# Kernel optimization log

Hardware: AMD Instinct MI355X
Metric: run time of the kernel (lower is better)

Reference implementation:

```python
import jax, jax.numpy as jnp
import numpy as np

ALPHA = 1.702  # sigmoid-GLU scale
LIMIT = 7.0    # clamp limit
TOP_K = 2      # num_experts_per_tok


def setup_inputs() -> dict:
    key = jax.random.key(0)
    ks = jax.random.split(key, 4)
    B, S, H, E, I = 2, 1024, 1024, 8, 2048
    return {
        "hidden_states": jax.random.normal(ks[0], (B, S, H), jnp.float32),
        "router_weight": jax.random.normal(ks[1], (E, H), jnp.float32),
        "router_bias": jnp.zeros((E,), jnp.float32),
        "gate_up_proj": jax.random.normal(ks[2], (E, H, 2 * I), jnp.float32) * 0.02,
        "gate_up_bias": jnp.zeros((E, 2 * I), jnp.float32),
        "down_proj": jax.random.normal(ks[3], (E, I, H), jnp.float32) * 0.02,
        "down_bias": jnp.zeros((E, H), jnp.float32),
    }


def reference(hidden_states, router_weight, router_bias, gate_up_proj,
              gate_up_bias, down_proj, down_bias):
    B, S, H = hidden_states.shape
    E, _, two_I = gate_up_proj.shape
    I = two_I // 2

    flat = hidden_states.reshape(B * S, H)  # [T, H]

    # Router: softmax + top-k
    logits = flat @ router_weight.T + router_bias            # [T, E]
    scores = jax.nn.softmax(logits, axis=-1)
    topk_w, topk_idx = jax.lax.top_k(scores, TOP_K)          # [T, K]

    # Dense per-expert gated FFN (einsum 'abmh,ehn->abemn' computes all experts
    # on all tokens; the reshape/permute dance is a mathematical no-op).
    gu = jnp.einsum('th,ehn->ten', flat, gate_up_proj) + gate_up_bias  # [T, E, 2I]
    gate = jnp.minimum(gu[..., :I], LIMIT)
    up = jnp.clip(gu[..., I:], -LIMIT, LIMIT)
    glu = gate * jax.nn.sigmoid(gate * ALPHA)
    act = (up + 1.0) * glu                                   # [T, E, I]

    down = jnp.einsum('tei,eih->teh', act, down_proj) + down_bias  # [T, E, H]

    # Combine: gather each token's top-k expert outputs, weighted sum.
    gathered = jnp.take_along_axis(down, topk_idx[:, :, None], axis=1)  # [T, K, H]
    out = (gathered * topk_w[:, :, None]).sum(axis=1)        # [T, H]
    return out.reshape(B, S, H)
```

## Files before the change

kernel.cpp:

```cpp
#include <hip/hip_runtime.h>
#include <math.h>

#define TT 2048
#define HH 1024
#define EE 8
#define II 2048
#define N1 4096
#define ALPHA 1.702f
#define LIMIT 7.0f
#define MAXSCHED 40

typedef __attribute__((ext_vector_type(8))) short short8;
typedef __attribute__((ext_vector_type(4))) float floatx4;

#define GLL(g, l) __builtin_amdgcn_global_load_lds(                          \
    (const __attribute__((address_space(1))) void*)(g),                      \
    (__attribute__((address_space(3))) void*)(l), 16, 0, 0)

__device__ __forceinline__ short f2bf(float f) {
  union { float f; unsigned u; } v; v.f = f;
  unsigned r = (v.u + 0x7fffu + ((v.u >> 16) & 1u)) >> 16;
  return (short)r;
}
__device__ __forceinline__ float bf2f(unsigned short s) {
  union { unsigned u; float f; } v; v.u = ((unsigned)s) << 16;
  return v.f;
}

__global__ __launch_bounds__(256) void convert_x(const float* __restrict__ x,
                                                 unsigned short* __restrict__ xb) {
  const size_t off = ((size_t)blockIdx.x * blockDim.x + threadIdx.x) * 8;
  const float4 v0 = *(const float4*)(x + off);
  const float4 v1 = *(const float4*)(x + off + 4);
  short8 s;
  s[0]=f2bf(v0.x); s[1]=f2bf(v0.y); s[2]=f2bf(v0.z); s[3]=f2bf(v0.w);
  s[4]=f2bf(v1.x); s[5]=f2bf(v1.y); s[6]=f2bf(v1.z); s[7]=f2bf(v1.w);
  *(short8*)(xb + off) = s;
}

__global__ __launch_bounds__(256) void router_kernel(
    const float* __restrict__ x, const float* __restrict__ rw,
    const float* __restrict__ rb, int* __restrict__ topk_idx,
    float* __restrict__ topk_w) {
  const int t = blockIdx.x;
  const float* xr = x + (size_t)t * HH;
  const int lane = threadIdx.x & 63;
  const int wave = threadIdx.x >> 6;
  float xv[16];
#pragma unroll
  for (int i = 0; i < 16; i++) xv[i] = xr[lane + i * 64];
  __shared__ float logits[EE];
#pragma unroll
  for (int ee = 0; ee < 2; ee++) {
    const int e = wave * 2 + ee;
    const float* wr = rw + (size_t)e * HH;
    float s = 0.f;
#pragma unroll
    for (int i = 0; i < 16; i++) s += xv[i] * wr[lane + i * 64];
#pragma unroll
    for (int off = 32; off > 0; off >>= 1) s += __shfl_down(s, off, 64);
    if (lane == 0) logits[e] = s + rb[e];
  }
  __syncthreads();
  if (threadIdx.x == 0) {
    float sc[EE];
    float mx = -3.4e38f;
    for (int i = 0; i < EE; i++) mx = fmaxf(mx, logits[i]);
    float sum = 0.f;
    for (int i = 0; i < EE; i++) { sc[i] = expf(logits[i] - mx); sum += sc[i]; }
    const float inv = 1.f / sum;
    int i0 = 0;
    for (int i = 1; i < EE; i++) if (sc[i] > sc[i0]) i0 = i;
    int i1 = (i0 == 0) ? 1 : 0;
    for (int i = 0; i < EE; i++) if (i != i0 && sc[i] > sc[i1]) i1 = i;
    topk_idx[t * 2 + 0] = i0;
    topk_idx[t * 2 + 1] = i1;
    topk_w[t * 2 + 0] = sc[i0] * inv;
    topk_w[t * 2 + 1] = sc[i1] * inv;
  }
}

__global__ void assign_kernel(const int* __restrict__ topk_idx,
                              int* __restrict__ counts, int* __restrict__ rows) {
  const int id = blockIdx.x * blockDim.x + threadIdx.x;
  if (id >= TT * 2) return;
  const int e = topk_idx[id];
  const int slot = atomicAdd(&counts[e], 1);
  rows[e * TT + slot] = id;
}

__global__ void sched_kernel(const int* __restrict__ counts,
                             int* __restrict__ sched, int* __restrict__ nsched) {
  if (threadIdx.x == 0) {
    int n = 0;
    for (int e = 0; e < EE; e++) {
      const int mt = (counts[e] + 127) >> 7;
      for (int m = 0; m < mt; m++) sched[n++] = (e << 8) | m;
    }
    nsched[0] = n;
  }
}

__global__ __launch_bounds__(256, 3) void gemm_gu(
    const unsigned short* __restrict__ x_bf,
    const float* __restrict__ gup,
    const float* __restrict__ gub,
    const int* __restrict__ counts, const int* __restrict__ rows,
    const int* __restrict__ sched, const int* __restrict__ nsched,
    unsigned short* __restrict__ gu) {
  const int sid = blockIdx.y;
  if (sid >= nsched[0]) return;
  const int sv = sched[sid];
  const int e = sv >> 8, mtile = sv & 255;
  const int count = counts[e] - mtile * 128;
  const int ntile = blockIdx.x;
  const int* rl = rows + e * TT + mtile * 128;

  __shared__ short As[128 * 128];

  const int tid = threadIdx.x;
  const int lane = tid & 63, wave = tid >> 6;
  const int quad = lane >> 4, r16 = lane & 15;
  const int wm = (wave & 1) << 6, wn = (wave >> 1) << 6;

  const unsigned short* asrc[8];
#pragma unroll
  for (int p = 0; p < 8; p++) {
    const int m = wave * 32 + p * 4 + (lane >> 4);
    const int cm = (m < count) ? m : 0;
    const int g = (lane & 15) ^ (m & 15);
    asrc[p] = x_bf + (size_t)(rl[cm] >> 1) * HH + g * 8;
  }

  const int nbase = ntile * 128 + wn + r16;
  int voff[8];
#pragma unroll
  for (int j = 0; j < 8; j++) voff[j] = (quad * 8 + j) * N1 + nbase;
  const float* bbase = gup + (size_t)e * HH * N1;

  floatx4 acc[4][4] = {};

  for (int c = 0; c < 8; c++) {
    __syncthreads();
#pragma unroll
    for (int p = 0; p < 8; p++)
      GLL(asrc[p] + c * 128, &As[(wave * 32 + p * 4) * 128]);
    __syncthreads();
#pragma unroll 2
    for (int kt = 0; kt < 4; kt++) {
      short8 af[4];
#pragma unroll
      for (int i = 0; i < 4; i++) {
        const int m = wm + i * 16 + r16;
        const int sl = (kt * 4 + quad) ^ r16;
        af[i] = *(const short8*)&As[m * 128 + sl * 8];
      }
#pragma unroll
      for (int f = 0; f < 4; f++) {
        float bv[8];
#pragma unroll
        for (int j = 0; j < 8; j++) bv[j] = bbase[voff[j] + f * 16];
        union { unsigned u[4]; short8 s8; } bp;
#pragma unroll
        for (int j = 0; j < 4; j++)
          bp.u[j] = __builtin_amdgcn_perm(__float_as_uint(bv[2 * j + 1]),
                                          __float_as_uint(bv[2 * j]), 0x07060302u);
#pragma unroll
        for (int i = 0; i < 4; i++)
          acc[i][f] = __builtin_amdgcn_mfma_f32_16x16x32_bf16(af[i], bp.s8, acc[i][f], 0, 0, 0);
      }
#pragma unroll
      for (int j = 0; j < 8; j++) voff[j] += 32 * N1;
    }
  }

  const float* bias = gub + (size_t)e * N1 + ntile * 128;
#pragma unroll
  for (int i = 0; i < 4; i++) {
#pragma unroll
    for (int reg = 0; reg < 4; reg++) {
      const int rrow = wm + i * 16 + quad * 4 + reg;
      if (rrow < count) {
        const int ent = rl[rrow];
        unsigned short* orow = gu + (size_t)ent * N1 + ntile * 128;
#pragma unroll
        for (int f = 0; f < 4; f++) {
          const int cc = wn + f * 16 + r16;
          orow[cc] = (unsigned short)f2bf(acc[i][f][reg] + bias[cc]);
        }
      }
    }
  }
}

__global__ __launch_bounds__(256) void act_kernel(const unsigned short* __restrict__ gu,
                                                  unsigned short* __restrict__ act) {
  const int id = blockIdx.x * blockDim.x + threadIdx.x;
  const int r = id >> 8;
  const int i8 = (id & 255) * 8;
  const short8 g8 = *(const short8*)(gu + (size_t)r * N1 + i8);
  const short8 u8 = *(const short8*)(gu + (size_t)r * N1 + II + i8);
  short8 o;
#pragma unroll
  for (int j = 0; j < 8; j++) {
    float g = bf2f((unsigned short)g8[j]);
    float u = bf2f((unsigned short)u8[j]);
    g = fminf(g, LIMIT);
    u = fminf(fmaxf(u, -LIMIT), LIMIT);
    const float glu = g / (1.f + expf(-g * ALPHA));
    o[j] = f2bf((u + 1.f) * glu);
  }
  *(short8*)(act + (size_t)r * II + i8) = o;
}

__global__ __launch_bounds__(256, 3) void gemm_down(
    const unsigned short* __restrict__ act,
    const float* __restrict__ dp,
    const int* __restrict__ counts, const int* __restrict__ rows,
    const int* __restrict__ sched, const int* __restrict__ nsched,
    float* __restrict__ dout) {
  const int sid = blockIdx.y;
  if (sid >= nsched[0]) return;
  const int sv = sched[sid];
  const int e = sv >> 8, mtile = sv & 255;
  const int count = counts[e] - mtile * 128;
  const int ntile = blockIdx.x;
  const int kbase = blockIdx.z * (II / 4);
  const int* rl = rows + e * TT + mtile * 128;

  __shared__ short As[128 * 128];

  const int tid = threadIdx.x;
  const int lane = tid & 63, wave = tid >> 6;
  const int quad = lane >> 4, r16 = lane & 15;
  const int wm = (wave & 1) << 6, wn = (wave >> 1) << 6;

  const unsigned short* asrc[8];
#pragma unroll
  for (int p = 0; p < 8; p++) {
    const int m = wave * 32 + p * 4 + (lane >> 4);
    const int cm = (m < count) ? m : 0;
    const int g = (lane & 15) ^ (m & 15);
    asrc[p] = act + (size_t)rl[cm] * II + kbase + g * 8;
  }

  const int nbase = ntile * 128 + wn + r16;
  int voff[8];
#pragma unroll
  for (int j = 0; j < 8; j++) voff[j] = (kbase + quad * 8 + j) * HH + nbase;
  const float* bbase = dp + (size_t)e * II * HH;

  floatx4 acc[4][4] = {};

  for (int c = 0; c < 4; c++) {
    __syncthreads();
#pragma unroll
    for (int p = 0; p < 8; p++)
      GLL(asrc[p] + c * 128, &As[(wave * 32 + p * 4) * 128]);
    __syncthreads();
#pragma unroll 2
    for (int kt = 0; kt < 4; kt++) {
      short8 af[4];
#pragma unroll
      for (int i = 0; i < 4; i++) {
        const int m = wm + i * 16 + r16;
        const int sl = (kt * 4 + quad) ^ r16;
        af[i] = *(const short8*)&As[m * 128 + sl * 8];
      }
#pragma unroll
      for (int f = 0; f < 4; f++) {
        float bv[8];
#pragma unroll
        for (int j = 0; j < 8; j++) bv[j] = bbase[voff[j] + f * 16];
        union { unsigned u[4]; short8 s8; } bp;
#pragma unroll
        for (int j = 0; j < 4; j++)
          bp.u[j] = __builtin_amdgcn_perm(__float_as_uint(bv[2 * j + 1]),
                                          __float_as_uint(bv[2 * j]), 0x07060302u);
#pragma unroll
        for (int i = 0; i < 4; i++)
          acc[i][f] = __builtin_amdgcn_mfma_f32_16x16x32_bf16(af[i], bp.s8, acc[i][f], 0, 0, 0);
      }
#pragma unroll
      for (int j = 0; j < 8; j++) voff[j] += 32 * HH;
    }
  }

#pragma unroll
  for (int i = 0; i < 4; i++) {
#pragma unroll
    for (int reg = 0; reg < 4; reg++) {
      const int rrow = wm + i * 16 + quad * 4 + reg;
      if (rrow < count) {
        const int ent = rl[rrow];
        float* orow = dout + (size_t)ent * HH + ntile * 128;
#pragma unroll
        for (int f = 0; f < 4; f++) {
          const int cc = wn + f * 16 + r16;
          atomicAdd(&orow[cc], acc[i][f][reg]);
        }
      }
    }
  }
}

__global__ __launch_bounds__(256) void combine_kernel(
    const float* __restrict__ dout, const float* __restrict__ tw,
    const int* __restrict__ tidx, const float* __restrict__ db,
    float* __restrict__ out) {
  const int id = blockIdx.x * blockDim.x + threadIdx.x;
  const int t = id >> 8;
  const int h = (id & 255) * 4;
  const float w0 = tw[t * 2], w1 = tw[t * 2 + 1];
  const int e0 = tidx[t * 2], e1 = tidx[t * 2 + 1];
  const float4 a = *(const float4*)(dout + (size_t)(2 * t) * HH + h);
  const float4 b = *(const float4*)(dout + (size_t)(2 * t + 1) * HH + h);
  const float4 b0 = *(const float4*)(db + (size_t)e0 * HH + h);
  const float4 b1 = *(const float4*)(db + (size_t)e1 * HH + h);
  float4 o;
  o.x = w0 * (a.x + b0.x) + w1 * (b.x + b1.x);
  o.y = w0 * (a.y + b0.y) + w1 * (b.y + b1.y);
  o.z = w0 * (a.z + b0.z) + w1 * (b.z + b1.z);
  o.w = w0 * (a.w + b0.w) + w1 * (b.w + b1.w);
  *(float4*)(out + (size_t)t * HH + h) = o;
}

extern "C" void kernel_launch(void* const* d_in, const int* in_sizes, int n_in,
                              void* d_out, int out_size, void* d_ws, size_t ws_size,
                              hipStream_t stream) {
  const float* x   = (const float*)d_in[0];
  const float* rw  = (const float*)d_in[1];
  const float* rb  = (const float*)d_in[2];
  const float* gup = (const float*)d_in[3];
  const float* gub = (const float*)d_in[4];
  const float* dp  = (const float*)d_in[5];
  const float* db  = (const float*)d_in[6];
  float* out = (float*)d_out;

  char* ws = (char*)d_ws;
  int*   topk_idx = (int*)(ws + 0);
  float* topk_w   = (float*)(ws + 16384);
  int*   counts   = (int*)(ws + 32768);
  int*   nsched   = (int*)(ws + 33024);
  int*   sched    = (int*)(ws + 33280);
  int*   rows     = (int*)(ws + 36864);
  unsigned short* x_bf = (unsigned short*)(ws + (1u << 20));
  unsigned short* gu   = (unsigned short*)(ws + 8388608);
  unsigned short* act  = (unsigned short*)(ws + 50331648);
  float*          dout = (float*)(ws + 75497472);

  convert_x<<<TT * HH / (256 * 8), 256, 0, stream>>>(x, x_bf);
  router_kernel<<<TT, 256, 0, stream>>>(x, rw, rb, topk_idx, topk_w);
  hipMemsetAsync(counts, 0, 64, stream);
  assign_kernel<<<(TT * 2 + 255) / 256, 256, 0, stream>>>(topk_idx, counts, rows);
  sched_kernel<<<1, 64, 0, stream>>>(counts, sched, nsched);
  gemm_gu<<<dim3(N1 / 128, MAXSCHED), 256, 0, stream>>>(
      x_bf, gup, gub, counts, rows, sched, nsched, gu);
  act_kernel<<<TT * 2 * II / (256 * 8), 256, 0, stream>>>(gu, act);
  hipMemsetAsync(dout, 0, (size_t)TT * 2 * HH * 4, stream);
  gemm_down<<<dim3(HH / 128, MAXSCHED, 4), 256, 0, stream>>>(
      act, dp, counts, rows, sched, nsched, dout);
  combine_kernel<<<(TT * HH / 4) / 256, 256, 0, stream>>>(dout, topk_w, topk_idx, db, out);
}
```

Before: 457.2 us.

## Fuse GLU activation into gate-up GEMM, use 32x32 MFMA, drop split-K atomics

The gate-up GEMM now tiles 64 gate columns and the matching 64 up columns together, so the clamp and sigmoid-GLU run in its epilogue. This removes the separate activation kernel and the bf16 round-trip of the gate/up buffer. Both GEMMs switch from 16x16x32 to 32x32x16 bf16 MFMA with a 2x2 accumulator layout. Split-K partials in the down GEMM are written to separate slices and summed in the combine kernel, replacing atomics and the memset at the cost of more combine-time memory reads. Occupancy hints rise to 4 blocks per SIMD group.

After: 495.0 us. 8.3% more time.

```diff
diff --git a/kernel.cpp b/kernel.cpp
--- a/kernel.cpp
+++ b/kernel.cpp
@@ -9,9 +9,10 @@
 #define ALPHA 1.702f
 #define LIMIT 7.0f
 #define MAXSCHED 40
+#define SPLITK 4
 
 typedef __attribute__((ext_vector_type(8))) short short8;
-typedef __attribute__((ext_vector_type(4))) float floatx4;
+typedef __attribute__((ext_vector_type(16))) float floatx16;
 
 #define GLL(g, l) __builtin_amdgcn_global_load_lds(                          \
     (const __attribute__((address_space(1))) void*)(g),                      \
@@ -101,13 +102,13 @@
   }
 }
 
-__global__ __launch_bounds__(256, 3) void gemm_gu(
+__global__ __launch_bounds__(256, 4) void gemm_gu(
     const unsigned short* __restrict__ x_bf,
     const float* __restrict__ gup,
     const float* __restrict__ gub,
     const int* __restrict__ counts, const int* __restrict__ rows,
     const int* __restrict__ sched, const int* __restrict__ nsched,
-    unsigned short* __restrict__ gu) {
+    unsigned short* __restrict__ act) {
   const int sid = blockIdx.y;
   if (sid >= nsched[0]) return;
   const int sv = sched[sid];
@@ -120,8 +121,9 @@
 
   const int tid = threadIdx.x;
   const int lane = tid & 63, wave = tid >> 6;
-  const int quad = lane >> 4, r16 = lane & 15;
-  const int wm = (wave & 1) << 6, wn = (wave >> 1) << 6;
+  const int half = lane >> 5, n32 = lane & 31;
+  const int wm = (wave & 1) << 6;
+  const int wh = (wave >> 1) << 5;
 
   const unsigned short* asrc[8];
 #pragma unroll
@@ -132,13 +134,11 @@
     asrc[p] = x_bf + (size_t)(rl[cm] >> 1) * HH + g * 8;
   }
 
-  const int nbase = ntile * 128 + wn + r16;
-  int voff[8];
-#pragma unroll
-  for (int j = 0; j < 8; j++) voff[j] = (quad * 8 + j) * N1 + nbase;
+  const int acol = wh + n32;
+  const int colf[2] = { ntile * 64 + acol, II + ntile * 64 + acol };
   const float* bbase = gup + (size_t)e * HH * N1;
 
-  floatx4 acc[4][4] = {};
+  floatx16 acc[2][2] = {};
 
   for (int c = 0; c < 8; c++) {
     __syncthreads();
@@ -147,73 +147,53 @@
       GLL(asrc[p] + c * 128, &As[(wave * 32 + p * 4) * 128]);
     __syncthreads();
 #pragma unroll 2
-    for (int kt = 0; kt < 4; kt++) {
-      short8 af[4];
-#pragma unroll
-      for (int i = 0; i < 4; i++) {
-        const int m = wm + i * 16 + r16;
-        const int sl = (kt * 4 + quad) ^ r16;
+    for (int kt = 0; kt < 8; kt++) {
+      short8 af[2];
+#pragma unroll
+      for (int i = 0; i < 2; i++) {
+        const int m = wm + i * 32 + n32;
+        const int sl = (kt * 2 + half) ^ (m & 15);
         af[i] = *(const short8*)&As[m * 128 + sl * 8];
       }
-#pragma unroll
-      for (int f = 0; f < 4; f++) {
+      const float* bp0 = bbase + (size_t)(c * 128 + kt * 16 + half * 8) * N1;
+#pragma unroll
+      for (int nf = 0; nf < 2; nf++) {
         float bv[8];
 #pragma unroll
-        for (int j = 0; j < 8; j++) bv[j] = bbase[voff[j] + f * 16];
+        for (int j = 0; j < 8; j++) bv[j] = bp0[j * N1 + colf[nf]];
         union { unsigned u[4]; short8 s8; } bp;
 #pragma unroll
         for (int j = 0; j < 4; j++)
           bp.u[j] = __builtin_amdgcn_perm(__float_as_uint(bv[2 * j + 1]),
                                           __float_as_uint(bv[2 * j]), 0x07060302u);
 #pragma unroll
-        for (int i = 0; i < 4; i++)
-          acc[i][f] = __builtin_amdgcn_mfma_f32_16x16x32_bf16(af[i], bp.s8, acc[i][f], 0, 0, 0);
-      }
-#pragma unroll
-      for (int j = 0; j < 8; j++) voff[j] += 32 * N1;
-    }
-  }
-
-  const float* bias = gub + (size_t)e * N1 + ntile * 128;
-#pragma unroll
-  for (int i = 0; i < 4; i++) {
-#pragma unroll
-    for (int reg = 0; reg < 4; reg++) {
-      const int rrow = wm + i * 16 + quad * 4 + reg;
-      if (rrow < count) {
-        const int ent = rl[rrow];
-        unsigned short* orow = gu + (size_t)ent * N1 + ntile * 128;
-#pragma unroll
-        for (int f = 0; f < 4; f++) {
-          const int cc = wn + f * 16 + r16;
-          orow[cc] = (unsigned short)f2bf(acc[i][f][reg] + bias[cc]);
-        }
-      }
-    }
-  }
-}
-
-__global__ __launch_bounds__(256) void act_kernel(const unsigned short* __restrict__ gu,
-                                                  unsigned short* __restrict__ act) {
-  const int id = blockIdx.x * blockDim.x + threadIdx.x;
-  const int r = id >> 8;
-  const int i8 = (id & 255) * 8;
-  const short8 g8 = *(const short8*)(gu + (size_t)r * N1 + i8);
-  const short8 u8 = *(const short8*)(gu + (size_t)r * N1 + II + i8);
-  short8 o;
-#pragma unroll
-  for (int j = 0; j < 8; j++) {
-    float g = bf2f((unsigned short)g8[j]);
-    float u = bf2f((unsigned short)u8[j]);
-    g = fminf(g, LIMIT);
-    u = fminf(fmaxf(u, -LIMIT), LIMIT);
-    const float glu = g / (1.f + expf(-g * ALPHA));
-    o[j] = f2bf((u + 1.f) * glu);
-  }
-  *(short8*)(act + (size_t)r * II + i8) = o;
-}
-
-__global__ __launch_bounds__(256, 3) void gemm_down(
+        for (int i = 0; i < 2; i++)
+          acc[i][nf] = __builtin_amdgcn_mfma_f32_32x32x16_bf16(af[i], bp.s8, acc[i][nf], 0, 0, 0);
+      }
+    }
+  }
+
+  const float bg = gub[(size_t)e * N1 + ntile * 64 + acol];
+  const float bu = gub[(size_t)e * N1 + II + ntile * 64 + acol];
+#pragma unroll
+  for (int i = 0; i < 2; i++) {
+#pragma unroll
+    for (int reg = 0; reg < 16; reg++) {
+      const int r = wm + i * 32 + (reg & 3) + 8 * (reg >> 2) + 4 * half;
+      if (r < count) {
+        const int ent = rl[r];
+        float g = acc[i][0][reg] + bg;
+        float u = acc[i][1][reg] + bu;
+        g = fminf(g, LIMIT);
+        u = fminf(fmaxf(u, -LIMIT), LIMIT);
+        const float glu = g / (1.f + expf(-g * ALPHA));
+        act[(size_t)ent * II + ntile * 64 + acol] = (unsigned short)f2bf((u + 1.f) * glu);
+      }
+    }
+  }
+}
+
+__global__ __launch_bounds__(256, 4) void gemm_down(
     const unsigned short* __restrict__ act,
     const float* __restrict__ dp,
     const int* __restrict__ counts, const int* __restrict__ rows,
@@ -225,15 +205,17 @@
   const int e = sv >> 8, mtile = sv & 255;
   const int count = counts[e] - mtile * 128;
   const int ntile = blockIdx.x;
-  const int kbase = blockIdx.z * (II / 4);
+  const int split = blockIdx.z;
+  const int kbase = split * (II / SPLITK);
   const int* rl = rows + e * TT + mtile * 128;
 
   __shared__ short As[128 * 128];
 
   const int tid = threadIdx.x;
   const int lane = tid & 63, wave = tid >> 6;
-  const int quad = lane >> 4, r16 = lane & 15;
-  const int wm = (wave & 1) << 6, wn = (wave >> 1) << 6;
+  const int half = lane >> 5, n32 = lane & 31;
+  const int wm = (wave & 1) << 6;
+  const int wn = (wave >> 1) << 6;
 
   const unsigned short* asrc[8];
 #pragma unroll
@@ -244,61 +226,55 @@
     asrc[p] = act + (size_t)rl[cm] * II + kbase + g * 8;
   }
 
-  const int nbase = ntile * 128 + wn + r16;
-  int voff[8];
-#pragma unroll
-  for (int j = 0; j < 8; j++) voff[j] = (kbase + quad * 8 + j) * HH + nbase;
+  const int colf[2] = { ntile * 128 + wn + n32, ntile * 128 + wn + 32 + n32 };
   const float* bbase = dp + (size_t)e * II * HH;
 
-  floatx4 acc[4][4] = {};
-
-  for (int c = 0; c < 4; c++) {
+  floatx16 acc[2][2] = {};
+
+  for (int c = 0; c < II / SPLITK / 128; c++) {
     __syncthreads();
 #pragma unroll
     for (int p = 0; p < 8; p++)
       GLL(asrc[p] + c * 128, &As[(wave * 32 + p * 4) * 128]);
     __syncthreads();
 #pragma unroll 2
-    for (int kt = 0; kt < 4; kt++) {
-      short8 af[4];
-#pragma unroll
-      for (int i = 0; i < 4; i++) {
-        const int m = wm + i * 16 + r16;
-        const int sl = (kt * 4 + quad) ^ r16;
+    for (int kt = 0; kt < 8; kt++) {
+      short8 af[2];
+#pragma unroll
+      for (int i = 0; i < 2; i++) {
+        const int m = wm + i * 32 + n32;
+        const int sl = (kt * 2 + half) ^ (m & 15);
         af[i] = *(const short8*)&As[m * 128 + sl * 8];
       }
-#pragma unroll
-      for (int f = 0; f < 4; f++) {
+      const float* bp0 = bbase + (size_t)(kbase + c * 128 + kt * 16 + half * 8) * HH;
+#pragma unroll
+      for (int nf = 0; nf < 2; nf++) {
         float bv[8];
 #pragma unroll
-        for (int j = 0; j < 8; j++) bv[j] = bbase[voff[j] + f * 16];
+        for (int j = 0; j < 8; j++) bv[j] = bp0[j * HH + colf[nf]];
         union { unsigned u[4]; short8 s8; } bp;
 #pragma unroll
         for (int j = 0; j < 4; j++)
           bp.u[j] = __builtin_amdgcn_perm(__float_as_uint(bv[2 * j + 1]),
                                           __float_as_uint(bv[2 * j]), 0x07060302u);
 #pragma unroll
-        for (int i = 0; i < 4; i++)
-          acc[i][f] = __builtin_amdgcn_mfma_f32_16x16x32_bf16(af[i], bp.s8, acc[i][f], 0, 0, 0);
-      }
-#pragma unroll
-      for (int j = 0; j < 8; j++) voff[j] += 32 * HH;
-    }
-  }
-
-#pragma unroll
-  for (int i = 0; i < 4; i++) {
-#pragma unroll
-    for (int reg = 0; reg < 4; reg++) {
-      const int rrow = wm + i * 16 + quad * 4 + reg;
-      if (rrow < count) {
-        const int ent = rl[rrow];
-        float* orow = dout + (size_t)ent * HH + ntile * 128;
-#pragma unroll
-        for (int f = 0; f < 4; f++) {
-          const int cc = wn + f * 16 + r16;
-          atomicAdd(&orow[cc], acc[i][f][reg]);
-        }
+        for (int i = 0; i < 2; i++)
+          acc[i][nf] = __builtin_amdgcn_mfma_f32_32x32x16_bf16(af[i], bp.s8, acc[i][nf], 0, 0, 0);
+      }
+    }
+  }
+
+  float* dsl = dout + (size_t)split * (TT * 2) * HH;
+#pragma unroll
+  for (int i = 0; i < 2; i++) {
+#pragma unroll
+    for (int reg = 0; reg < 16; reg++) {
+      const int r = wm + i * 32 + (reg & 3) + 8 * (reg >> 2) + 4 * half;
+      if (r < count) {
+        const int ent = rl[r];
+#pragma unroll
+        for (int nf = 0; nf < 2; nf++)
+          dsl[(size_t)ent * HH + colf[nf]] = acc[i][nf][reg];
       }
     }
   }
@@ -311,17 +287,21 @@
   const int id = blockIdx.x * blockDim.x + threadIdx.x;
   const int t = id >> 8;
   const int h = (id & 255) * 4;
-  const float w0 = tw[t * 2], w1 = tw[t * 2 + 1];
-  const int e0 = tidx[t * 2], e1 = tidx[t * 2 + 1];
-  const float4 a = *(const float4*)(dout + (size_t)(2 * t) * HH + h);
-  const float4 b = *(const float4*)(dout + (size_t)(2 * t + 1) * HH + h);
-  const float4 b0 = *(const float4*)(db + (size_t)e0 * HH + h);
-  const float4 b1 = *(const float4*)(db + (size_t)e1 * HH + h);
-  float4 o;
-  o.x = w0 * (a.x + b0.x) + w1 * (b.x + b1.x);
-  o.y = w0 * (a.y + b0.y) + w1 * (b.y + b1.y);
-  o.z = w0 * (a.z + b0.z) + w1 * (b.z + b1.z);
-  o.w = w0 * (a.w + b0.w) + w1 * (b.w + b1.w);
+  float4 o = {0.f, 0.f, 0.f, 0.f};
+#pragma unroll
+  for (int k = 0; k < 2; k++) {
+    const float w = tw[t * 2 + k];
+    const int e = tidx[t * 2 + k];
+    const float4 bb = *(const float4*)(db + (size_t)e * HH + h);
+    float4 s = bb;
+#pragma unroll
+    for (int sp = 0; sp < SPLITK; sp++) {
+      const float4 d = *(const float4*)(dout +
+          ((size_t)sp * (TT * 2) + t * 2 + k) * HH + h);
+      s.x += d.x; s.y += d.y; s.z += d.z; s.w += d.w;
+    }
+    o.x += w * s.x; o.y += w * s.y; o.z += w * s.z; o.w += w * s.w;
+  }
   *(float4*)(out + (size_t)t * HH + h) = o;
 }
 
@@ -345,20 +325,17 @@
   int*   sched    = (int*)(ws + 33280);
   int*   rows     = (int*)(ws + 36864);
   unsigned short* x_bf = (unsigned short*)(ws + (1u << 20));
-  unsigned short* gu   = (unsigned short*)(ws + 8388608);
-  unsigned short* act  = (unsigned short*)(ws + 50331648);
-  float*          dout = (float*)(ws + 75497472);
+  unsigned short* act  = (unsigned short*)(ws + 6291456);
+  float*          dout = (float*)(ws + 23068672);
 
   convert_x<<<TT * HH / (256 * 8), 256, 0, stream>>>(x, x_bf);
   router_kernel<<<TT, 256, 0, stream>>>(x, rw, rb, topk_idx, topk_w);
   hipMemsetAsync(counts, 0, 64, stream);
   assign_kernel<<<(TT * 2 + 255) / 256, 256, 0, stream>>>(topk_idx, counts, rows);
   sched_kernel<<<1, 64, 0, stream>>>(counts, sched, nsched);
-  gemm_gu<<<dim3(N1 / 128, MAXSCHED), 256, 0, stream>>>(
-      x_bf, gup, gub, counts, rows, sched, nsched, gu);
-  act_kernel<<<TT * 2 * II / (256 * 8), 256, 0, stream>>>(gu, act);
-  hipMemsetAsync(dout, 0, (size_t)TT * 2 * HH * 4, stream);
-  gemm_down<<<dim3(HH / 128, MAXSCHED, 4), 256, 0, stream>>>(
+  gemm_gu<<<dim3(II / 64, MAXSCHED), 256, 0, stream>>>(
+      x_bf, gup, gub, counts, rows, sched, nsched, act);
+  gemm_down<<<dim3(HH / 128, MAXSCHED, SPLITK), 256, 0, stream>>>(
       act, dp, counts, rows, sched, nsched, dout);
   combine_kernel<<<(TT * HH / 4) / 256, 256, 0, stream>>>(dout, topk_w, topk_idx, db, out);
 }
```
